# Performance work log

Measured on AMD Instinct MI355X. Metric: run time of the kernel, lower is better.

## Reference

```python
import jax, jax.numpy as jnp
import numpy as np

H = 1024
EPS = 1e-5
MIX_SCALE = 0.1


def setup_inputs() -> dict:
    key = jax.random.key(0)
    ks = jax.random.split(key, 6)
    B, S = 8, 4096
    x = jax.random.normal(ks[0], (B, S, H), dtype=jnp.float32)
    # to_complex: Linear(H, 2H); store weight as [H, 2H] for x @ W
    W_to = jax.random.normal(ks[1], (H, 2 * H), dtype=jnp.float32) * (1.0 / np.sqrt(H))
    b_to = jax.random.normal(ks[2], (2 * H,), dtype=jnp.float32) * 0.01
    # from_complex: Linear(2H, H)
    W_from = jax.random.normal(ks[3], (2 * H, H), dtype=jnp.float32) * (1.0 / np.sqrt(2 * H))
    b_from = jax.random.normal(ks[4], (H,), dtype=jnp.float32) * 0.01
    phase_shifts = jnp.zeros((1, 1, H), dtype=jnp.float32)
    return {"x": x, "W_to": W_to, "b_to": b_to, "W_from": W_from,
            "b_from": b_from, "phase_shifts": phase_shifts}


def reference(x, W_to, b_to, W_from, b_from, phase_shifts):
    # x: [B,S,H]
    complex_repr = x @ W_to + b_to                      # [B,S,2H]
    real, imag = jnp.split(complex_repr, 2, axis=-1)    # each [B,S,H]
    magnitude = jnp.sqrt(real**2 + imag**2 + EPS)
    phase = jnp.arctan2(imag, real)                     # [B,S,H]
    # mean_j cos(phase_i - phase_j + shift)
    #   = cos(phase_i + shift) * mean_j cos(phase_j)
    #   + sin(phase_i + shift) * mean_j sin(phase_j)
    # (exact trig identity; replaces the [B,S,S,H] materialization)
    mean_cos = jnp.mean(jnp.cos(phase), axis=1, keepdims=True)  # [B,1,H]
    mean_sin = jnp.mean(jnp.sin(phase), axis=1, keepdims=True)  # [B,1,H]
    shifted = phase + phase_shifts                              # [B,S,H]
    mixed_phase = jnp.cos(shifted) * mean_cos + jnp.sin(shifted) * mean_sin
    new_phase = phase + mixed_phase * MIX_SCALE
    new_real = magnitude * jnp.cos(new_phase)
    new_imag = magnitude * jnp.sin(new_phase)
    new_complex = jnp.concatenate([new_real, new_imag], axis=-1)  # [B,S,2H]
    return new_complex @ W_from + b_from                          # [B,S,H]
```

## Files before the change

### kernel.cpp

```cpp
#include <hip/hip_runtime.h>
#include <hip/hip_bf16.h>
#include <math.h>

#define H 1024
#define N1 2048
#define BATCH 8
#define SEQ 4096
#define M_TOT (BATCH*SEQ)
#define EPS 1e-5f
#define MIX 0.1f

typedef __attribute__((ext_vector_type(8))) short bf16x8;
typedef __attribute__((ext_vector_type(4))) float f32x4;
typedef unsigned short ushort_t;
typedef unsigned int uint_t;

static __device__ __forceinline__ float bf2f(unsigned short u) {
    return __uint_as_float(((unsigned)u) << 16);
}
static __device__ __forceinline__ unsigned short f2bf(float x) {
    __hip_bfloat16 h = __float2bfloat16(x);
    return *reinterpret_cast<unsigned short*>(&h);
}
static __device__ __forceinline__ void gload16(const void* g, void* l) {
    __builtin_amdgcn_global_load_lds(
        (const __attribute__((address_space(1))) unsigned int*)g,
        (__attribute__((address_space(3))) unsigned int*)l,
        16, 0, 0);
}
static __device__ __forceinline__ int perm2h(int c)  { return ((c & 1023) << 1) | (c >> 10); }
static __device__ __forceinline__ int invperm(int k) { return (k >> 1) | ((k & 1) << 10); }

__global__ __launch_bounds__(256) void cvt_f32_bf16(
    const float* __restrict__ in, unsigned short* __restrict__ out, size_t n)
{
    size_t i = ((size_t)blockIdx.x * 256 + threadIdx.x) * 8;
    if (i >= n) return;
    float4 a = *(const float4*)(in + i);
    float4 b = *(const float4*)(in + i + 4);
    union { unsigned short u[8]; uint4 v; } p;
    p.u[0] = f2bf(a.x); p.u[1] = f2bf(a.y); p.u[2] = f2bf(a.z); p.u[3] = f2bf(a.w);
    p.u[4] = f2bf(b.x); p.u[5] = f2bf(b.y); p.u[6] = f2bf(b.z); p.u[7] = f2bf(b.w);
    *(uint4*)(out + i) = p.v;
}

__global__ __launch_bounds__(256) void transpose_wt(
    const float* __restrict__ in, unsigned short* __restrict__ out)
{
    __shared__ float tile[64][65];
    const int c0 = blockIdx.x * 64, r0 = blockIdx.y * 64;
    const int tc = threadIdx.x & 63, tr4 = (threadIdx.x >> 6) * 16;
    #pragma unroll
    for (int rr = 0; rr < 16; ++rr)
        tile[tr4 + rr][tc] = in[(size_t)(r0 + tr4 + rr) * N1 + c0 + tc];
    __syncthreads();
    #pragma unroll
    for (int rr = 0; rr < 16; ++rr)
        out[(size_t)perm2h(c0 + tr4 + rr) * H + r0 + tc] = f2bf(tile[tc][tr4 + rr]);
}

__global__ __launch_bounds__(256) void transpose_wf(
    const float* __restrict__ in, unsigned short* __restrict__ out)
{
    __shared__ float tile[64][65];
    const int n0 = blockIdx.x * 64, k0 = blockIdx.y * 64;
    const int tc = threadIdx.x & 63, tr4 = (threadIdx.x >> 6) * 16;
    #pragma unroll
    for (int rr = 0; rr < 16; ++rr)
        tile[tr4 + rr][tc] = in[(size_t)invperm(k0 + tr4 + rr) * H + n0 + tc];
    __syncthreads();
    #pragma unroll
    for (int rr = 0; rr < 16; ++rr)
        out[(size_t)(n0 + tr4 + rr) * N1 + k0 + tc] = f2bf(tile[tc][tr4 + rr]);
}

template<int KDIM>
static __device__ __forceinline__ void gemm_core(
    const unsigned short* __restrict__ A, const unsigned short* __restrict__ Bt,
    int m0, int n0, int t, unsigned short* As, unsigned short* Bs,
    f32x4 (&acc)[4][4])
{
    const int lane = t & 63;
    const int wid  = t >> 6;
    const int wr   = wid >> 1, wc = wid & 1;

    const int sr = t >> 2;
    const int sc = (t & 3) * 8;
    const unsigned short* Ag0 = A  + (size_t)(m0 + sr)      * KDIM + sc;
    const unsigned short* Ag1 = A  + (size_t)(m0 + 64 + sr) * KDIM + sc;
    const unsigned short* Bg0 = Bt + (size_t)(n0 + sr)      * KDIM + sc;
    const unsigned short* Bg1 = Bt + (size_t)(n0 + 64 + sr) * KDIM + sc;
    unsigned short* Al0 = &As[t * 8];
    unsigned short* Al1 = &As[2048 + t * 8];
    unsigned short* Bl0 = &Bs[t * 8];
    unsigned short* Bl1 = &Bs[2048 + t * 8];

    const int fr = lane & 15;
    const int kb = (lane >> 4) * 8;

    for (int k0 = 0; k0 < KDIM; k0 += 32) {
        gload16(Ag0 + k0, Al0);
        gload16(Ag1 + k0, Al1);
        gload16(Bg0 + k0, Bl0);
        gload16(Bg1 + k0, Bl1);
        __syncthreads();

        bf16x8 af[4], bfv[4];
        #pragma unroll
        for (int i = 0; i < 4; ++i)
            af[i] = *(const bf16x8*)&As[(wr * 64 + i * 16 + fr) * 32 + kb];
        #pragma unroll
        for (int j = 0; j < 4; ++j)
            bfv[j] = *(const bf16x8*)&Bs[(wc * 64 + j * 16 + fr) * 32 + kb];

        #pragma unroll
        for (int i = 0; i < 4; ++i)
            #pragma unroll
            for (int j = 0; j < 4; ++j)
                acc[i][j] = __builtin_amdgcn_mfma_f32_16x16x32_bf16(
                    af[i], bfv[j], acc[i][j], 0, 0, 0);
        __syncthreads();
    }
}

__global__ __launch_bounds__(256) void gemm1_mfma(
    const unsigned short* __restrict__ A, const unsigned short* __restrict__ Bt,
    const float* __restrict__ bt, unsigned short* __restrict__ c1,
    float* __restrict__ sums)
{
    __shared__ unsigned short As[128 * 32];
    __shared__ unsigned short Bs[128 * 32];

    const int t = threadIdx.x;
    const unsigned wg = ((blockIdx.x & 7) << 9) | (blockIdx.x >> 3);
    const int n0 = (wg & 15) * 128;
    const int m0 = (wg >> 4) * 128;

    f32x4 acc[4][4] = {};
    gemm_core<H>(A, Bt, m0, n0, t, As, Bs, acc);

    const int lane = t & 63;
    const int wid  = t >> 6;
    const int wr   = wid >> 1, wc = wid & 1;
    const int fr   = lane & 15;
    const int rbase = (lane >> 4) * 4;

    #pragma unroll
    for (int j = 0; j < 4; ++j) {
        const int n = n0 + wc * 64 + j * 16 + fr;
        const float bb = bt[invperm(n)];
        #pragma unroll
        for (int i = 0; i < 4; ++i)
            #pragma unroll
            for (int r = 0; r < 4; ++r)
                acc[i][j][r] += bb;
    }

    #pragma unroll
    for (int i = 0; i < 4; ++i)
        #pragma unroll
        for (int j = 0; j < 4; ++j) {
            const int col = n0 + wc * 64 + j * 16 + fr;
            #pragma unroll
            for (int r = 0; r < 4; ++r) {
                const size_t row = (size_t)(m0 + wr * 64 + i * 16 + rbase + r);
                c1[row * N1 + col] = f2bf(acc[i][j][r]);
            }
        }

    float lc[4] = {0, 0, 0, 0}, ls[4] = {0, 0, 0, 0};
    #pragma unroll
    for (int j = 0; j < 4; ++j)
        #pragma unroll
        for (int i = 0; i < 4; ++i)
            #pragma unroll
            for (int r = 0; r < 4; ++r) {
                const float own = acc[i][j][r];
                const float oth = __shfl_xor(own, 1);
                const float re = (fr & 1) ? oth : own;
                const float im = (fr & 1) ? own : oth;
                const float rsq = rsqrtf(fmaxf(re * re + im * im, 1e-30f));
                lc[j] += re * rsq;
                ls[j] += im * rsq;
            }
    #pragma unroll
    for (int j = 0; j < 4; ++j) {
        lc[j] += __shfl_xor(lc[j], 16); lc[j] += __shfl_xor(lc[j], 32);
        ls[j] += __shfl_xor(ls[j], 16); ls[j] += __shfl_xor(ls[j], 32);
    }
    if (lane < 16 && !(lane & 1)) {
        const int b = m0 >> 12;
        #pragma unroll
        for (int j = 0; j < 4; ++j) {
            const int h = (n0 + wc * 64 + j * 16 + fr) >> 1;
            atomicAdd(&sums[(b * 2 + 0) * H + h], lc[j]);
            atomicAdd(&sums[(b * 2 + 1) * H + h], ls[j]);
        }
    }
}

__global__ __launch_bounds__(256) void gemm2_mfma(
    const unsigned short* __restrict__ A, const unsigned short* __restrict__ Bt,
    const float* __restrict__ bf, float* __restrict__ out)
{
    __shared__ unsigned short As[128 * 32];
    __shared__ unsigned short Bs[128 * 32];

    const int t = threadIdx.x;
    const unsigned wg = ((blockIdx.x & 7) << 8) | (blockIdx.x >> 3);
    const int n0 = (wg & 7) * 128;
    const int m0 = (wg >> 3) * 128;

    f32x4 acc[4][4] = {};
    gemm_core<N1>(A, Bt, m0, n0, t, As, Bs, acc);

    const int lane = t & 63;
    const int wid  = t >> 6;
    const int wr   = wid >> 1, wc = wid & 1;
    const int fr   = lane & 15;
    const int rbase = (lane >> 4) * 4;

    #pragma unroll
    for (int i = 0; i < 4; ++i)
        #pragma unroll
        for (int j = 0; j < 4; ++j) {
            const int col = n0 + wc * 64 + j * 16 + fr;
            const float bb = bf[col];
            #pragma unroll
            for (int r = 0; r < 4; ++r) {
                const size_t row = (size_t)(m0 + wr * 64 + i * 16 + rbase + r);
                out[row * H + col] = acc[i][j][r] + bb;
            }
        }
}

__global__ void finalize_pq(const float* __restrict__ sums, const float* __restrict__ ps,
                            float* __restrict__ P, float* __restrict__ Q)
{
    int i = blockIdx.x * 256 + threadIdx.x;
    int b = i >> 10, h = i & (H - 1);
    float mc = sums[(b * 2 + 0) * H + h] * (1.0f / SEQ);
    float ms = sums[(b * 2 + 1) * H + h] * (1.0f / SEQ);
    float cp = cosf(ps[h]), sp = sinf(ps[h]);
    P[i] = mc * cp + ms * sp;
    Q[i] = ms * cp - mc * sp;
}

__global__ __launch_bounds__(256) void phase_mix(
    unsigned short* __restrict__ c1, const float* __restrict__ P,
    const float* __restrict__ Q)
{
    const size_t total = (size_t)M_TOT * N1 / 8;
    for (size_t q = (size_t)blockIdx.x * 256 + threadIdx.x; q < total;
         q += (size_t)gridDim.x * 256) {
        const size_t m = q >> 8;
        const int off = ((int)q & 255) * 8;
        const int b = (int)(m >> 12);
        const int h0 = off >> 1;
        uint4* cu = (uint4*)c1;
        const size_t idx = ((size_t)m * N1 + off) >> 3;
        uint4 v = cu[idx];
        float4 Pv = *(const float4*)&P[b * H + h0];
        float4 Qv = *(const float4*)&Q[b * H + h0];
        const uint_t w[4] = { v.x, v.y, v.z, v.w };
        const float Pk[4] = { Pv.x, Pv.y, Pv.z, Pv.w };
        const float Qk[4] = { Qv.x, Qv.y, Qv.z, Qv.w };
        uint_t o[4];
        #pragma unroll
        for (int e = 0; e < 4; ++e) {
            float r  = bf2f(w[e] & 0xffff);
            float im = bf2f(w[e] >> 16);
            float tt = r * r + im * im;
            float minv = rsqrtf(fmaxf(tt, 1e-30f));
            float d = MIX * (r * Pk[e] + im * Qk[e]) * minv;
            float d2 = d * d;
            float cd = 1.0f - d2 * (0.5f - d2 * (1.0f / 24.0f));
            float sd = d * (1.0f - d2 * ((1.0f / 6.0f) - d2 * (1.0f / 120.0f)));
            float sc = sqrtf(tt + EPS) * minv;
            o[e] = (uint_t)f2bf(sc * (r * cd - im * sd))
                 | ((uint_t)f2bf(sc * (im * cd + r * sd)) << 16);
        }
        v.x = o[0]; v.y = o[1]; v.z = o[2]; v.w = o[3];
        cu[idx] = v;
    }
}

extern "C" void kernel_launch(void* const* d_in, const int* in_sizes, int n_in,
                              void* d_out, int out_size, void* d_ws, size_t ws_size,
                              hipStream_t stream) {
    const float* x  = (const float*)d_in[0];
    const float* Wt = (const float*)d_in[1];
    const float* bt = (const float*)d_in[2];
    const float* Wf = (const float*)d_in[3];
    const float* bf = (const float*)d_in[4];
    const float* ps = (const float*)d_in[5];
    float* out = (float*)d_out;

    const size_t c1_bytes   = (size_t)M_TOT * N1 * 2;
    const size_t wft_bytes  = (size_t)H * N1 * 2;
    const size_t sums_bytes = (size_t)BATCH * 2 * H * 4;
    const size_t pq_bytes   = (size_t)BATCH * H * 4;
    if (ws_size < c1_bytes + wft_bytes + sums_bytes + 2 * pq_bytes) return;

    unsigned short* c1  = (unsigned short*)d_ws;
    unsigned short* WfT = (unsigned short*)((char*)d_ws + c1_bytes);
    float* sums = (float*)((char*)d_ws + c1_bytes + wft_bytes);
    float* Pb   = (float*)((char*)d_ws + c1_bytes + wft_bytes + sums_bytes);
    float* Qb   = (float*)((char*)d_ws + c1_bytes + wft_bytes + sums_bytes + pq_bytes);

    unsigned short* xb  = (unsigned short*)d_out;
    unsigned short* WtT = (unsigned short*)d_out + (size_t)M_TOT * H;

    hipMemsetAsync(sums, 0, sums_bytes, stream);

    cvt_f32_bf16<<<dim3((unsigned)(((size_t)M_TOT * H / 8 + 255) / 256)), 256, 0, stream>>>(
        x, xb, (size_t)M_TOT * H);
    transpose_wt<<<dim3(N1 / 64, H / 64), 256, 0, stream>>>(Wt, WtT);
    transpose_wf<<<dim3(H / 64, N1 / 64), 256, 0, stream>>>(Wf, WfT);

    gemm1_mfma<<<dim3(4096), 256, 0, stream>>>(xb, WtT, bt, c1, sums);

    finalize_pq<<<dim3(BATCH * H / 256), 256, 0, stream>>>(sums, ps, Pb, Qb);
    phase_mix<<<dim3(4096), 256, 0, stream>>>(c1, Pb, Qb);

    gemm2_mfma<<<dim3(2048), 256, 0, stream>>>(c1, WfT, bf, out);
}
```

Baseline: 438.4 us.

## Replace both GEMMs with 256x256 double-buffered, LDS-swizzled 8-wave MFMA kernel

Replaces the simple 128x128, K=32, single-buffered GEMM core with a templated 512-thread kernel that computes 256x256 tiles. It stages K=64 chunks into double-buffered, XOR-swizzled LDS through async global-to-LDS loads, splits the K loop into phases that interleave prefetch with MFMA work, and uses explicit waitcnt, barriers and setprio. The aim is to hide global memory latency, raise data reuse per tile and avoid LDS bank conflicts. The cost is much higher LDS and register use (128 KB LDS per block, 8x4 accumulator fragments), and correctness depends on carefully hand-coded vmcnt accounting.

```diff
diff --git a/kernel.cpp b/kernel.cpp
--- a/kernel.cpp
+++ b/kernel.cpp
@@ -12,7 +12,6 @@
 
 typedef __attribute__((ext_vector_type(8))) short bf16x8;
 typedef __attribute__((ext_vector_type(4))) float f32x4;
-typedef unsigned short ushort_t;
 typedef unsigned int uint_t;
 
 static __device__ __forceinline__ float bf2f(unsigned short u) {
@@ -29,7 +28,6 @@
         16, 0, 0);
 }
 static __device__ __forceinline__ int perm2h(int c)  { return ((c & 1023) << 1) | (c >> 10); }
-static __device__ __forceinline__ int invperm(int k) { return (k >> 1) | ((k & 1) << 10); }
 
 __global__ __launch_bounds__(256) void cvt_f32_bf16(
     const float* __restrict__ in, unsigned short* __restrict__ out, size_t n)
@@ -66,172 +64,173 @@
     const int n0 = blockIdx.x * 64, k0 = blockIdx.y * 64;
     const int tc = threadIdx.x & 63, tr4 = (threadIdx.x >> 6) * 16;
     #pragma unroll
-    for (int rr = 0; rr < 16; ++rr)
-        tile[tr4 + rr][tc] = in[(size_t)invperm(k0 + tr4 + rr) * H + n0 + tc];
+    for (int rr = 0; rr < 16; ++rr) {
+        const int k = k0 + tr4 + rr;
+        tile[tr4 + rr][tc] = in[(size_t)((k >> 1) | ((k & 1) << 10)) * H + n0 + tc];
+    }
     __syncthreads();
     #pragma unroll
     for (int rr = 0; rr < 16; ++rr)
         out[(size_t)(n0 + tr4 + rr) * N1 + k0 + tc] = f2bf(tile[tc][tr4 + rr]);
 }
 
-template<int KDIM>
-static __device__ __forceinline__ void gemm_core(
-    const unsigned short* __restrict__ A, const unsigned short* __restrict__ Bt,
-    int m0, int n0, int t, unsigned short* As, unsigned short* Bs,
-    f32x4 (&acc)[4][4])
-{
+#define VM4 asm volatile("s_waitcnt vmcnt(4)" ::: "memory")
+#define VM0 asm volatile("s_waitcnt vmcnt(0)" ::: "memory")
+
+#define STG(X, BB, HH, CC, TT) \
+    gload16(X##g + (size_t)((HH)*128 + (CC)*64) * KDIM + (TT)*64, \
+            &X##s[BB][(HH)*8192 + (CC)*4096 + t*8])
+#define STAGE_HT(X, BB, HH, TT) do { STG(X, BB, HH, 0, TT); STG(X, BB, HH, 1, TT); } while(0)
+
+#define LDA(BB, MF, KS) (*(const bf16x8*)&As[BB][(wr*128 + (MF)*16 + fr)*64 + ((((KS)*4 + lg) ^ rsw))*8])
+#define LDB(BB, NF, KS) (*(const bf16x8*)&Bs[BB][(wc*64  + (NF)*16 + fr)*64 + ((((KS)*4 + lg) ^ rsw))*8])
+
+#define PHASE(BB, Q, STAGE_STMT, VM_STMT) do {                                  \
+    if ((Q) == 0) {                                                             \
+        _Pragma("unroll")                                                       \
+        for (int nf = 0; nf < 4; ++nf) {                                        \
+            bfr[nf][0] = LDB(BB, nf, 0);                                        \
+            bfr[nf][1] = LDB(BB, nf, 1);                                        \
+        }                                                                       \
+    }                                                                           \
+    afr[0][0] = LDA(BB, 2*(Q),   0); afr[0][1] = LDA(BB, 2*(Q),   1);           \
+    afr[1][0] = LDA(BB, 2*(Q)+1, 0); afr[1][1] = LDA(BB, 2*(Q)+1, 1);           \
+    STAGE_STMT;                                                                 \
+    __builtin_amdgcn_s_barrier();                                               \
+    asm volatile("s_waitcnt lgkmcnt(0)" ::: "memory");                          \
+    __builtin_amdgcn_sched_barrier(0);                                          \
+    __builtin_amdgcn_s_setprio(1);                                              \
+    _Pragma("unroll")                                                           \
+    for (int nf = 0; nf < 4; ++nf) {                                            \
+        acc[2*(Q)][nf]   = __builtin_amdgcn_mfma_f32_16x16x32_bf16(afr[0][0], bfr[nf][0], acc[2*(Q)][nf],   0,0,0); \
+        acc[2*(Q)][nf]   = __builtin_amdgcn_mfma_f32_16x16x32_bf16(afr[0][1], bfr[nf][1], acc[2*(Q)][nf],   0,0,0); \
+        acc[2*(Q)+1][nf] = __builtin_amdgcn_mfma_f32_16x16x32_bf16(afr[1][0], bfr[nf][0], acc[2*(Q)+1][nf], 0,0,0); \
+        acc[2*(Q)+1][nf] = __builtin_amdgcn_mfma_f32_16x16x32_bf16(afr[1][1], bfr[nf][1], acc[2*(Q)+1][nf], 0,0,0); \
+    }                                                                           \
+    __builtin_amdgcn_s_setprio(0);                                              \
+    VM_STMT;                                                                    \
+    __builtin_amdgcn_s_barrier();                                               \
+} while (0)
+
+template<int KDIM, bool G1>
+__global__ __launch_bounds__(512, 2) void gemm8(
+    const unsigned short* __restrict__ A,
+    const unsigned short* __restrict__ Bt,
+    const float* __restrict__ bias,
+    void* __restrict__ Cout,
+    float* __restrict__ sums)
+{
+    __shared__ __align__(16) unsigned short As[2][16384];
+    __shared__ __align__(16) unsigned short Bs[2][16384];
+
+    const int t    = threadIdx.x;
     const int lane = t & 63;
     const int wid  = t >> 6;
-    const int wr   = wid >> 1, wc = wid & 1;
-
-    const int sr = t >> 2;
-    const int sc = (t & 3) * 8;
-    const unsigned short* Ag0 = A  + (size_t)(m0 + sr)      * KDIM + sc;
-    const unsigned short* Ag1 = A  + (size_t)(m0 + 64 + sr) * KDIM + sc;
-    const unsigned short* Bg0 = Bt + (size_t)(n0 + sr)      * KDIM + sc;
-    const unsigned short* Bg1 = Bt + (size_t)(n0 + 64 + sr) * KDIM + sc;
-    unsigned short* Al0 = &As[t * 8];
-    unsigned short* Al1 = &As[2048 + t * 8];
-    unsigned short* Bl0 = &Bs[t * 8];
-    unsigned short* Bl1 = &Bs[2048 + t * 8];
-
-    const int fr = lane & 15;
-    const int kb = (lane >> 4) * 8;
-
-    for (int k0 = 0; k0 < KDIM; k0 += 32) {
-        gload16(Ag0 + k0, Al0);
-        gload16(Ag1 + k0, Al1);
-        gload16(Bg0 + k0, Bl0);
-        gload16(Bg1 + k0, Bl1);
-        __syncthreads();
-
-        bf16x8 af[4], bfv[4];
+    const int wr   = wid >> 2;
+    const int wc   = wid & 3;
+
+    int m0, n0;
+    if (G1) {
+        const unsigned wg = ((blockIdx.x & 7) << 7) | (blockIdx.x >> 3);
+        n0 = (wg & 7) * 256;
+        m0 = (wg >> 3) * 256;
+    } else {
+        const unsigned wg = ((blockIdx.x & 7) << 6) | (blockIdx.x >> 3);
+        n0 = (wg & 3) * 256;
+        m0 = (wg >> 2) * 256;
+    }
+
+    const int srow = t >> 3;
+    const int ssw  = ((srow >> 1) & 1) | (((srow >> 2) & 1) << 1);
+    const int gk   = ((t & 7) ^ ssw) * 8;
+    const unsigned short* Ag = A  + (size_t)(m0 + srow) * KDIM + gk;
+    const unsigned short* Bg = Bt + (size_t)(n0 + srow) * KDIM + gk;
+
+    const int fr  = lane & 15;
+    const int lg  = lane >> 4;
+    const int rsw = ((fr >> 1) & 1) | (((fr >> 2) & 1) << 1);
+
+    f32x4 acc[8][4] = {};
+    bf16x8 bfr[4][2];
+    bf16x8 afr[2][2];
+
+    constexpr int NITER = KDIM / 128;
+
+    STAGE_HT(A, 0, 0, 0); STAGE_HT(A, 0, 1, 0);
+    STAGE_HT(B, 0, 0, 0); STAGE_HT(B, 0, 1, 0);
+    STAGE_HT(B, 1, 0, 1); STAGE_HT(B, 1, 1, 1);
+    VM4;
+    __builtin_amdgcn_s_barrier();
+
+    for (int it = 0; it < NITER; ++it) {
+        const int  T1   = 2 * it + 1;
+        const int  T2   = 2 * it + 2;
+        const int  T3   = 2 * it + 3;
+        const bool more = (it + 1 < NITER);
+        PHASE(0, 0, STAGE_HT(A, 1, 0, T1), );
+        PHASE(0, 1, STAGE_HT(A, 1, 1, T1), );
+        PHASE(0, 2, if (more) STAGE_HT(B, 0, 0, T2), );
+        PHASE(0, 3, if (more) STAGE_HT(B, 0, 1, T2), if (more) { VM4; } else { VM0; });
+        PHASE(1, 0, if (more) STAGE_HT(A, 0, 0, T2), );
+        PHASE(1, 1, if (more) STAGE_HT(A, 0, 1, T2), );
+        PHASE(1, 2, if (more) STAGE_HT(B, 1, 0, T3), );
+        PHASE(1, 3, if (more) STAGE_HT(B, 1, 1, T3), if (more) { VM4; });
+    }
+
+    const int colbase = n0 + wc * 64;
+    if (G1) {
+        unsigned short* c1 = (unsigned short*)Cout;
+        float lc[4] = {0, 0, 0, 0}, ls[4] = {0, 0, 0, 0};
         #pragma unroll
-        for (int i = 0; i < 4; ++i)
-            af[i] = *(const bf16x8*)&As[(wr * 64 + i * 16 + fr) * 32 + kb];
+        for (int nf = 0; nf < 4; ++nf) {
+            const int col = colbase + nf * 16 + fr;
+            const float bb = bias[(col >> 1) | ((col & 1) << 10)];
+            #pragma unroll
+            for (int mf = 0; mf < 8; ++mf) {
+                #pragma unroll
+                for (int r = 0; r < 4; ++r) {
+                    const float v = acc[mf][nf][r] + bb;
+                    const size_t row = (size_t)(m0 + wr * 128 + mf * 16 + lg * 4 + r);
+                    c1[row * N1 + col] = f2bf(v);
+                    const float oth = __shfl_xor(v, 1);
+                    const float re = (fr & 1) ? oth : v;
+                    const float im = (fr & 1) ? v : oth;
+                    const float rq = rsqrtf(fmaxf(re * re + im * im, 1e-30f));
+                    lc[nf] += re * rq;
+                    ls[nf] += im * rq;
+                }
+            }
+        }
         #pragma unroll
-        for (int j = 0; j < 4; ++j)
-            bfv[j] = *(const bf16x8*)&Bs[(wc * 64 + j * 16 + fr) * 32 + kb];
-
+        for (int nf = 0; nf < 4; ++nf) {
+            lc[nf] += __shfl_xor(lc[nf], 16); lc[nf] += __shfl_xor(lc[nf], 32);
+            ls[nf] += __shfl_xor(ls[nf], 16); ls[nf] += __shfl_xor(ls[nf], 32);
+        }
+        if (lane < 16 && !(lane & 1)) {
+            const int b = m0 >> 12;
+            #pragma unroll
+            for (int nf = 0; nf < 4; ++nf) {
+                const int hh = (colbase + nf * 16 + fr) >> 1;
+                atomicAdd(&sums[(b * 2 + 0) * H + hh], lc[nf]);
+                atomicAdd(&sums[(b * 2 + 1) * H + hh], ls[nf]);
+            }
+        }
+    } else {
+        float* o = (float*)Cout;
         #pragma unroll
-        for (int i = 0; i < 4; ++i)
+        for (int nf = 0; nf < 4; ++nf) {
+            const int col = colbase + nf * 16 + fr;
+            const float bb = bias[col];
             #pragma unroll
-            for (int j = 0; j < 4; ++j)
-                acc[i][j] = __builtin_amdgcn_mfma_f32_16x16x32_bf16(
-                    af[i], bfv[j], acc[i][j], 0, 0, 0);
-        __syncthreads();
-    }
-}
-
-__global__ __launch_bounds__(256) void gemm1_mfma(
-    const unsigned short* __restrict__ A, const unsigned short* __restrict__ Bt,
-    const float* __restrict__ bt, unsigned short* __restrict__ c1,
-    float* __restrict__ sums)
-{
-    __shared__ unsigned short As[128 * 32];
-    __shared__ unsigned short Bs[128 * 32];
-
-    const int t = threadIdx.x;
-    const unsigned wg = ((blockIdx.x & 7) << 9) | (blockIdx.x >> 3);
-    const int n0 = (wg & 15) * 128;
-    const int m0 = (wg >> 4) * 128;
-
-    f32x4 acc[4][4] = {};
-    gemm_core<H>(A, Bt, m0, n0, t, As, Bs, acc);
-
-    const int lane = t & 63;
-    const int wid  = t >> 6;
-    const int wr   = wid >> 1, wc = wid & 1;
-    const int fr   = lane & 15;
-    const int rbase = (lane >> 4) * 4;
-
-    #pragma unroll
-    for (int j = 0; j < 4; ++j) {
-        const int n = n0 + wc * 64 + j * 16 + fr;
-        const float bb = bt[invperm(n)];
-        #pragma unroll
-        for (int i = 0; i < 4; ++i)
-            #pragma unroll
-            for (int r = 0; r < 4; ++r)
-                acc[i][j][r] += bb;
-    }
-
-    #pragma unroll
-    for (int i = 0; i < 4; ++i)
-        #pragma unroll
-        for (int j = 0; j < 4; ++j) {
-            const int col = n0 + wc * 64 + j * 16 + fr;
-            #pragma unroll
-            for (int r = 0; r < 4; ++r) {
-                const size_t row = (size_t)(m0 + wr * 64 + i * 16 + rbase + r);
-                c1[row * N1 + col] = f2bf(acc[i][j][r]);
+            for (int mf = 0; mf < 8; ++mf) {
+                #pragma unroll
+                for (int r = 0; r < 4; ++r) {
+                    const size_t row = (size_t)(m0 + wr * 128 + mf * 16 + lg * 4 + r);
+                    o[row * H + col] = acc[mf][nf][r] + bb;
+                }
             }
         }
-
-    float lc[4] = {0, 0, 0, 0}, ls[4] = {0, 0, 0, 0};
-    #pragma unroll
-    for (int j = 0; j < 4; ++j)
-        #pragma unroll
-        for (int i = 0; i < 4; ++i)
-            #pragma unroll
-            for (int r = 0; r < 4; ++r) {
-                const float own = acc[i][j][r];
-                const float oth = __shfl_xor(own, 1);
-                const float re = (fr & 1) ? oth : own;
-                const float im = (fr & 1) ? own : oth;
-                const float rsq = rsqrtf(fmaxf(re * re + im * im, 1e-30f));
-                lc[j] += re * rsq;
-                ls[j] += im * rsq;
-            }
-    #pragma unroll
-    for (int j = 0; j < 4; ++j) {
-        lc[j] += __shfl_xor(lc[j], 16); lc[j] += __shfl_xor(lc[j], 32);
-        ls[j] += __shfl_xor(ls[j], 16); ls[j] += __shfl_xor(ls[j], 32);
-    }
-    if (lane < 16 && !(lane & 1)) {
-        const int b = m0 >> 12;
-        #pragma unroll
-        for (int j = 0; j < 4; ++j) {
-            const int h = (n0 + wc * 64 + j * 16 + fr) >> 1;
-            atomicAdd(&sums[(b * 2 + 0) * H + h], lc[j]);
-            atomicAdd(&sums[(b * 2 + 1) * H + h], ls[j]);
-        }
-    }
-}
-
-__global__ __launch_bounds__(256) void gemm2_mfma(
-    const unsigned short* __restrict__ A, const unsigned short* __restrict__ Bt,
-    const float* __restrict__ bf, float* __restrict__ out)
-{
-    __shared__ unsigned short As[128 * 32];
-    __shared__ unsigned short Bs[128 * 32];
-
-    const int t = threadIdx.x;
-    const unsigned wg = ((blockIdx.x & 7) << 8) | (blockIdx.x >> 3);
-    const int n0 = (wg & 7) * 128;
-    const int m0 = (wg >> 3) * 128;
-
-    f32x4 acc[4][4] = {};
-    gemm_core<N1>(A, Bt, m0, n0, t, As, Bs, acc);
-
-    const int lane = t & 63;
-    const int wid  = t >> 6;
-    const int wr   = wid >> 1, wc = wid & 1;
-    const int fr   = lane & 15;
-    const int rbase = (lane >> 4) * 4;
-
-    #pragma unroll
-    for (int i = 0; i < 4; ++i)
-        #pragma unroll
-        for (int j = 0; j < 4; ++j) {
-            const int col = n0 + wc * 64 + j * 16 + fr;
-            const float bb = bf[col];
-            #pragma unroll
-            for (int r = 0; r < 4; ++r) {
-                const size_t row = (size_t)(m0 + wr * 64 + i * 16 + rbase + r);
-                out[row * H + col] = acc[i][j][r] + bb;
-            }
-        }
+    }
 }
 
 __global__ void finalize_pq(const float* __restrict__ sums, const float* __restrict__ ps,
@@ -318,10 +317,10 @@
     transpose_wt<<<dim3(N1 / 64, H / 64), 256, 0, stream>>>(Wt, WtT);
     transpose_wf<<<dim3(H / 64, N1 / 64), 256, 0, stream>>>(Wf, WfT);
 
-    gemm1_mfma<<<dim3(4096), 256, 0, stream>>>(xb, WtT, bt, c1, sums);
+    gemm8<H, true><<<dim3(1024), 512, 0, stream>>>(xb, WtT, bt, (void*)c1, sums);
 
     finalize_pq<<<dim3(BATCH * H / 256), 256, 0, stream>>>(sums, ps, Pb, Qb);
     phase_mix<<<dim3(4096), 256, 0, stream>>>(c1, Pb, Qb);
 
-    gemm2_mfma<<<dim3(2048), 256, 0, stream>>>(c1, WfT, bf, out);
-}
+    gemm8<N1, false><<<dim3(512), 512, 0, stream>>>(c1, WfT, bf, (void*)out, nullptr);
+}
```

Result: faster. 397.0 us (-9.4%).
